# Performance work log

Hardware: AMD Instinct MI355X
Metric: run time of the kernel (lower is better)

The kernel has to match this reference:

```python
import jax, jax.numpy as jnp
import numpy as np

IN_C, HID, L, NN, BS, OUT = 32, 128, 4, 64, 512, 3
N = NN * BS  # total graph vertices
EPS_LN = 1e-5
EPS_SM = 1e-16  # PyG softmax eps


def setup_inputs() -> dict:
    key = jax.random.key(0)
    ks = jax.random.split(key, 16)
    E = 524288
    x = jax.random.normal(ks[0], (N, IN_C), dtype=jnp.float32)
    edge_index = jax.random.randint(ks[1], (2, E), 0, N, dtype=jnp.int64)
    s = 0.1
    # first GAT layer (in -> hidden)
    W0 = jax.random.normal(ks[2], (IN_C, HID), dtype=jnp.float32) * s
    att_src0 = jax.random.normal(ks[3], (HID,), dtype=jnp.float32) * s
    att_dst0 = jax.random.normal(ks[4], (HID,), dtype=jnp.float32) * s
    bias0 = jnp.zeros((HID,), dtype=jnp.float32)
    # residual GAT layers (hidden -> hidden), stacked over L
    W_res = jax.random.normal(ks[5], (L, HID, HID), dtype=jnp.float32) * s
    att_src_res = jax.random.normal(ks[6], (L, HID), dtype=jnp.float32) * s
    att_dst_res = jax.random.normal(ks[7], (L, HID), dtype=jnp.float32) * s
    bias_res = jnp.zeros((L, HID), dtype=jnp.float32)
    gamma = jnp.ones((L, HID), dtype=jnp.float32)
    beta = jnp.zeros((L, HID), dtype=jnp.float32)
    # per-node predictor heads
    W1p = jax.random.normal(ks[8], (NN, HID, HID // 2), dtype=jnp.float32) * s
    W2p = jax.random.normal(ks[9], (NN, HID // 2, OUT), dtype=jnp.float32) * s
    return {"x": x, "edge_index": edge_index, "W0": W0, "att_src0": att_src0,
            "att_dst0": att_dst0, "bias0": bias0, "W_res": W_res,
            "att_src_res": att_src_res, "att_dst_res": att_dst_res,
            "bias_res": bias_res, "gamma": gamma, "beta": beta,
            "W1p": W1p, "W2p": W2p}


def _gat(x, src, dst, W, a_src, a_dst, b):
    # PyG GATConv, heads=1, negative_slope=0.2, self-loops already appended
    h = x @ W                                   # [N, H]
    a_s = (h * a_src).sum(-1)                   # [N]
    a_d = (h * a_dst).sum(-1)                   # [N]
    e = jax.nn.leaky_relu(a_s[src] + a_d[dst], 0.2)   # [E]
    m = jax.ops.segment_max(e, dst, num_segments=N)
    e = jnp.exp(e - m[dst])
    z = jax.ops.segment_sum(e, dst, num_segments=N)
    alpha = e / (z[dst] + EPS_SM)               # [E]
    out = jax.ops.segment_sum(h[src] * alpha[:, None], dst, num_segments=N)
    return out + b


def _layernorm(x, g, b):
    mu = x.mean(-1, keepdims=True)
    var = ((x - mu) ** 2).mean(-1, keepdims=True)
    return (x - mu) * jax.lax.rsqrt(var + EPS_LN) * g + b


def reference(x, edge_index, W0, att_src0, att_dst0, bias0, W_res,
              att_src_res, att_dst_res, bias_res, gamma, beta, W1p, W2p):
    loops = jnp.arange(N, dtype=edge_index.dtype)
    src = jnp.concatenate([edge_index[0], loops])
    dst = jnp.concatenate([edge_index[1], loops])
    # first GAT + relu
    h = jax.nn.relu(_gat(x, src, dst, W0, att_src0, att_dst0, bias0))
    # res+ blocks: h = h + conv(dropout(act(norm(h))))  (dropout=identity, eval)
    for i in range(L):
        t = jax.nn.relu(_layernorm(h, gamma[i], beta[i]))
        t = _gat(t, src, dst, W_res[i], att_src_res[i], att_dst_res[i], bias_res[i])
        h = h + t
    h = jax.nn.relu(_layernorm(h, gamma[0], beta[0]))
    # per-node predictor heads
    h = h.reshape(NN, BS, HID)
    t = jax.nn.relu(jnp.einsum('nbh,nhk->nbk', h, W1p))
    logits = jnp.einsum('nbk,nko->nbo', t, W2p)
    return jax.nn.softmax(logits, axis=-1)   # softmax over class dim (dim=1 per node slice)
```

## Files before the change

### kernel.cpp

```cpp
#include <hip/hip_runtime.h>
#include <hip/hip_fp8.h>
#include <math.h>

#define NND   32768
#define HIDD  128
#define NHEAD 64
#define BSS   512
#define OUTC  3

typedef _Float16 half_t;
typedef __attribute__((ext_vector_type(8))) _Float16 half8;
typedef __attribute__((ext_vector_type(4))) float f32x4;

__device__ __forceinline__ unsigned enc_fp8x4(float a, float b, float c, float d) {
    __hip_fp8x4_e4m3 q(make_float4(a, b, c, d));
    return (unsigned)q.__x;
}
__device__ __forceinline__ float4 dec_fp8x4(unsigned v) {
    __hip_fp8x4_e4m3 t; t.__x = (__hip_fp8x4_storage_t)v;
    return (float4)t;
}

__global__ __launch_bounds__(256) void prep_kernel(const float* __restrict__ W0,
        const float* __restrict__ W_res, const float* __restrict__ W1p,
        const float* __restrict__ as0, const float* __restrict__ ad0,
        const float* __restrict__ as_res, const float* __restrict__ ad_res,
        const float* __restrict__ x, const int* __restrict__ ei, int E,
        half_t* __restrict__ Wh, half_t* __restrict__ W1h, half_t* __restrict__ W0t,
        float* __restrict__ wvec, half_t* __restrict__ xh,
        int* __restrict__ counts, int* __restrict__ rank) {
    int b = blockIdx.x, tid = threadIdx.x;
    if (b < 64) {
        __shared__ float tile[32][33];
        int l = b >> 4, t = b & 15;
        int k0 = (t >> 2) * 32, n0 = (t & 3) * 32;
        const float* src = W_res + (size_t)l * 128 * 128;
        half_t* dst = Wh + (size_t)l * 128 * 128;
        int c = tid & 31, r0 = tid >> 5;
#pragma unroll
        for (int i = 0; i < 4; ++i) tile[r0 + i * 8][c] = src[(size_t)(k0 + r0 + i * 8) * 128 + n0 + c];
        __syncthreads();
#pragma unroll
        for (int i = 0; i < 4; ++i) dst[(size_t)(n0 + r0 + i * 8) * 128 + k0 + c] = (half_t)tile[c][r0 + i * 8];
    } else if (b < 576) {
        __shared__ float tile[32][33];
        int bb = b - 64, head = bb >> 3, t = bb & 7;
        int k0 = (t >> 1) * 32, n0 = (t & 1) * 32;
        const float* src = W1p + (size_t)head * 128 * 64;
        half_t* dst = W1h + (size_t)head * 64 * 128;
        int c = tid & 31, r0 = tid >> 5;
#pragma unroll
        for (int i = 0; i < 4; ++i) tile[r0 + i * 8][c] = src[(size_t)(k0 + r0 + i * 8) * 64 + n0 + c];
        __syncthreads();
#pragma unroll
        for (int i = 0; i < 4; ++i) dst[(size_t)(n0 + r0 + i * 8) * 128 + k0 + c] = (half_t)tile[c][r0 + i * 8];
    } else if (b == 576) {
        __shared__ float t0[32][129];
        for (int i = tid; i < 4096; i += 256) t0[i >> 7][i & 127] = W0[i];
        __syncthreads();
        for (int i = tid; i < 4096; i += 256) { int n = i >> 5, k = i & 31; W0t[n * 32 + k] = (half_t)t0[k][n]; }
    } else if (b == 577) {
        for (int task = tid; task < 1088; task += 256) {
            const float* row; const float* att; int slot, sd;
            if (task < 64) {
                int k = task >> 1; sd = task & 1;
                row = W0 + k * 128; att = sd ? ad0 : as0; slot = k;
            } else {
                int tt = task - 64; int l = 1 + tt / 256; int r = tt % 256;
                int k = r >> 1; sd = r & 1;
                row = W_res + (size_t)(l - 1) * 16384 + k * 128;
                att = (sd ? ad_res : as_res) + (l - 1) * 128;
                slot = l * 128 + k;
            }
            float s = 0.f;
            for (int n = 0; n < 128; ++n) s += row[n] * att[n];
            (sd ? wvec + 640 : wvec)[slot] = s;
        }
    } else if (b < 1090) {
        int b2 = b - 578;
        const float* xs = x + (size_t)b2 * 64 * 32;
        half_t* xd = xh + (size_t)b2 * 64 * 32;
        for (int i = tid; i < 1024; i += 256) {
            float2 v = ((const float2*)xs)[i];
            union { unsigned u; half_t h[2]; } cv;
            cv.h[0] = (half_t)v.x; cv.h[1] = (half_t)v.y;
            ((unsigned*)xd)[i] = cv.u;
        }
    } else {
        int j = (b - 1090) * 256 + tid;
        int Etot = E + NND;
        if (j >= Etot) return;
        int dst = (j < E) ? ei[E + j] : (j - E);
        rank[j] = atomicAdd(&counts[dst], 1);
    }
}

__global__ __launch_bounds__(1024) void scan_kernel(const int* __restrict__ counts,
                                                    int* __restrict__ off) {
    __shared__ int sums[1024];
    int tid = threadIdx.x;
    int base = tid * 32;
    int tmp[32];
    int run = 0;
#pragma unroll
    for (int i = 0; i < 8; ++i) {
        int4 c4 = *(const int4*)&counts[base + i * 4];
        tmp[i*4+0] = run; run += c4.x;
        tmp[i*4+1] = run; run += c4.y;
        tmp[i*4+2] = run; run += c4.z;
        tmp[i*4+3] = run; run += c4.w;
    }
    sums[tid] = run;
    __syncthreads();
    for (int d = 1; d < 1024; d <<= 1) {
        int v = (tid >= d) ? sums[tid - d] : 0;
        __syncthreads();
        sums[tid] += v;
        __syncthreads();
    }
    int ebase = (tid == 0) ? 0 : sums[tid - 1];
#pragma unroll
    for (int i = 0; i < 32; ++i) off[base + i] = ebase + tmp[i];
    if (tid == 1023) off[NND] = sums[1023];
}

__global__ __launch_bounds__(256) void fill_a0_kernel(const int* __restrict__ ei, int E, int egrid,
        const int* __restrict__ off, const int* __restrict__ rank, int* __restrict__ csr_src,
        const half_t* __restrict__ xh, const float* __restrict__ wvec,
        float* __restrict__ a_s, float* __restrict__ a_d) {
    int b = blockIdx.x, tid = threadIdx.x;
    if (b < egrid) {
        int j = b * 256 + tid;
        int Etot = E + NND;
        if (j >= Etot) return;
        int src, dst;
        if (j < E) { src = ei[j]; dst = ei[E + j]; }
        else       { src = j - E; dst = j - E; }
        csr_src[off[dst] + rank[j]] = src;
    } else {
        __shared__ float ws0[32], wd0[32];
        if (tid < 32) { ws0[tid] = wvec[tid]; wd0[tid] = wvec[640 + tid]; }
        __syncthreads();
        int g = (b - egrid) * 256 + tid;
        int node = g >> 2, part = g & 3;
        half8 xv = *(const half8*)&xh[(size_t)node * 32 + part * 8];
        float s = 0.f, d2 = 0.f;
#pragma unroll
        for (int j = 0; j < 8; ++j) { float f = (float)xv[j]; s += f * ws0[part * 8 + j]; d2 += f * wd0[part * 8 + j]; }
        s += __shfl_xor(s, 1); s += __shfl_xor(s, 2);
        d2 += __shfl_xor(d2, 1); d2 += __shfl_xor(d2, 2);
        if (part == 0) { a_s[node] = s; a_d[node] = d2; }
    }
}

__global__ __launch_bounds__(256) void agg0_kernel(const half_t* __restrict__ xh,
        const float* __restrict__ a_s, const float* __restrict__ a_dv,
        const int* __restrict__ csr_src, const int* __restrict__ off,
        half_t* __restrict__ P) {
    int d = (blockIdx.x * 256 + threadIdx.x) >> 6;
    int lane = threadIdx.x & 63;
    int q = lane >> 4, r15 = lane & 15;
    int beg = off[d], end = off[d + 1];
    float adv = a_dv[d];
    float pz = 0.f, a0 = 0.f, a1 = 0.f;
    for (int base = beg; base < end; base += 64) {
        int j = base + lane;
        int s = 0; float p = 0.f;
        if (j < end) {
            s = csr_src[j];
            float t = a_s[s] + adv;
            t = (t > 0.f) ? t : 0.2f * t;
            p = __expf(t);
        }
        pz += p;
        int cnt = end - base; if (cnt > 64) cnt = 64;
        int full = cnt & ~15;
        int k4 = 0;
        for (; k4 < full; k4 += 16) {
            int s0 = __shfl(s, k4 + q);      float p0 = __shfl(p, k4 + q);
            int s1 = __shfl(s, k4 + 4 + q);  float p1 = __shfl(p, k4 + 4 + q);
            int s2 = __shfl(s, k4 + 8 + q);  float p2 = __shfl(p, k4 + 8 + q);
            int s3 = __shfl(s, k4 + 12 + q); float p3 = __shfl(p, k4 + 12 + q);
            union { unsigned u; half_t h[2]; } u0, u1, u2, u3;
            u0.u = *(const unsigned*)&xh[(size_t)s0 * 32 + r15 * 2];
            u1.u = *(const unsigned*)&xh[(size_t)s1 * 32 + r15 * 2];
            u2.u = *(const unsigned*)&xh[(size_t)s2 * 32 + r15 * 2];
            u3.u = *(const unsigned*)&xh[(size_t)s3 * 32 + r15 * 2];
            a0 += p0 * (float)u0.h[0] + p1 * (float)u1.h[0] + p2 * (float)u2.h[0] + p3 * (float)u3.h[0];
            a1 += p0 * (float)u0.h[1] + p1 * (float)u1.h[1] + p2 * (float)u2.h[1] + p3 * (float)u3.h[1];
        }
        for (; k4 < cnt; k4 += 4) {
            int s0 = __shfl(s, k4 + q); float p0 = __shfl(p, k4 + q);
            union { unsigned u; half_t h[2]; } u0;
            u0.u = *(const unsigned*)&xh[(size_t)s0 * 32 + r15 * 2];
            a0 += p0 * (float)u0.h[0]; a1 += p0 * (float)u0.h[1];
        }
    }
#pragma unroll
    for (int o = 32; o; o >>= 1) pz += __shfl_xor(pz, o);
    a0 += __shfl_xor(a0, 16); a0 += __shfl_xor(a0, 32);
    a1 += __shfl_xor(a1, 16); a1 += __shfl_xor(a1, 32);
    if (q == 0) {
        float inv = 1.f / (pz + 1e-16f);
        union { unsigned u; half_t h[2]; } w;
        w.h[0] = (half_t)(a0 * inv); w.h[1] = (half_t)(a1 * inv);
        *(unsigned*)&P[(size_t)d * 32 + r15 * 2] = w.u;
    }
}

__global__ __launch_bounds__(256) void agg_kernel(const unsigned char* __restrict__ F8,
        const float* __restrict__ a_s, const float* __restrict__ a_dv,
        const int* __restrict__ csr_src, const int* __restrict__ off,
        half_t* __restrict__ P) {
    int d = (blockIdx.x * 256 + threadIdx.x) >> 6;
    int lane = threadIdx.x & 63;
    int q = lane >> 4, r15 = lane & 15;
    int beg = off[d], end = off[d + 1];
    float adv = a_dv[d];
    float pz = 0.f;
    float acc[8] = {0.f,0.f,0.f,0.f,0.f,0.f,0.f,0.f};
    for (int base = beg; base < end; base += 64) {
        int j = base + lane;
        int s = 0; float p = 0.f;
        if (j < end) {
            s = csr_src[j];
            float t = a_s[s] + adv;
            t = (t > 0.f) ? t : 0.2f * t;
            p = __expf(t);
        }
        pz += p;
        int cnt = end - base; if (cnt > 64) cnt = 64;
        int full = cnt & ~15;
        int k4 = 0;
        for (; k4 < full; k4 += 16) {
            int s0 = __shfl(s, k4 + q);      float p0 = __shfl(p, k4 + q);
            int s1 = __shfl(s, k4 + 4 + q);  float p1 = __shfl(p, k4 + 4 + q);
            int s2 = __shfl(s, k4 + 8 + q);  float p2 = __shfl(p, k4 + 8 + q);
            int s3 = __shfl(s, k4 + 12 + q); float p3 = __shfl(p, k4 + 12 + q);
            uint2 r0 = *(const uint2*)&F8[(size_t)s0 * HIDD + r15 * 8];
            uint2 r1 = *(const uint2*)&F8[(size_t)s1 * HIDD + r15 * 8];
            uint2 r2 = *(const uint2*)&F8[(size_t)s2 * HIDD + r15 * 8];
            uint2 r3 = *(const uint2*)&F8[(size_t)s3 * HIDD + r15 * 8];
            float4 f;
            f = dec_fp8x4(r0.x); acc[0]+=p0*f.x; acc[1]+=p0*f.y; acc[2]+=p0*f.z; acc[3]+=p0*f.w;
            f = dec_fp8x4(r0.y); acc[4]+=p0*f.x; acc[5]+=p0*f.y; acc[6]+=p0*f.z; acc[7]+=p0*f.w;
            f = dec_fp8x4(r1.x); acc[0]+=p1*f.x; acc[1]+=p1*f.y; acc[2]+=p1*f.z; acc[3]+=p1*f.w;
            f = dec_fp8x4(r1.y); acc[4]+=p1*f.x; acc[5]+=p1*f.y; acc[6]+=p1*f.z; acc[7]+=p1*f.w;
            f = dec_fp8x4(r2.x); acc[0]+=p2*f.x; acc[1]+=p2*f.y; acc[2]+=p2*f.z; acc[3]+=p2*f.w;
            f = dec_fp8x4(r2.y); acc[4]+=p2*f.x; acc[5]+=p2*f.y; acc[6]+=p2*f.z; acc[7]+=p2*f.w;
            f = dec_fp8x4(r3.x); acc[0]+=p3*f.x; acc[1]+=p3*f.y; acc[2]+=p3*f.z; acc[3]+=p3*f.w;
            f = dec_fp8x4(r3.y); acc[4]+=p3*f.x; acc[5]+=p3*f.y; acc[6]+=p3*f.z; acc[7]+=p3*f.w;
        }
        for (; k4 < cnt; k4 += 4) {
            int s0 = __shfl(s, k4 + q); float p0 = __shfl(p, k4 + q);
            uint2 r0 = *(const uint2*)&F8[(size_t)s0 * HIDD + r15 * 8];
            float4 f;
            f = dec_fp8x4(r0.x); acc[0]+=p0*f.x; acc[1]+=p0*f.y; acc[2]+=p0*f.z; acc[3]+=p0*f.w;
            f = dec_fp8x4(r0.y); acc[4]+=p0*f.x; acc[5]+=p0*f.y; acc[6]+=p0*f.z; acc[7]+=p0*f.w;
        }
    }
#pragma unroll
    for (int o = 32; o; o >>= 1) pz += __shfl_xor(pz, o);
#pragma unroll
    for (int i = 0; i < 8; ++i) {
        acc[i] += __shfl_xor(acc[i], 16);
        acc[i] += __shfl_xor(acc[i], 32);
    }
    if (q == 0) {
        float inv = 1.f / (pz + 1e-16f);
        union { int4 v; half_t hh[8]; } u;
#pragma unroll
        for (int i = 0; i < 8; ++i) u.hh[i] = (half_t)(acc[i] * inv);
        *(int4*)&P[(size_t)d * HIDD + r15 * 8] = u.v;
    }
}

template <int K, bool RES>
__global__ __launch_bounds__(256) void gemm_kernel(const half_t* __restrict__ P,
        const half_t* __restrict__ Whl, const float* __restrict__ bias,
        half_t* __restrict__ Hh, unsigned char* __restrict__ Th8,
        const float* __restrict__ gamma, const float* __restrict__ beta,
        const float* __restrict__ wsn, const float* __restrict__ wdn,
        float* __restrict__ a_s, float* __restrict__ a_d) {
    constexpr int KP = K + 8;
    constexpr int WB = 128 * KP * 2;
    constexpr int VB = 64 * 132 * 4;
    __shared__ __align__(16) char smraw[(WB > VB) ? WB : VB];
    half_t* w = (half_t*)smraw;
    float* vv = (float*)smraw;
    int tid = threadIdx.x;
    int n0 = blockIdx.x * 64;
    for (int i = tid; i < 128 * (K / 8); i += 256) {
        int n = i / (K / 8), c = i % (K / 8);
        *(int4*)&w[n * KP + c * 8] = *(const int4*)&Whl[(size_t)n * K + c * 8];
    }
    int wv = tid >> 6, lane = tid & 63;
    int q = lane >> 4, r15 = lane & 15;
    half8 afrag[K / 32];
    int nodeA = n0 + wv * 16 + r15;
#pragma unroll
    for (int s = 0; s < K / 32; ++s)
        afrag[s] = *(const half8*)&P[(size_t)nodeA * K + s * 32 + q * 8];
    __syncthreads();
    f32x4 acc[8];
#pragma unroll
    for (int ct = 0; ct < 8; ++ct) {
        f32x4 c = {0.f, 0.f, 0.f, 0.f};
#pragma unroll
        for (int s = 0; s < K / 32; ++s) {
            half8 bfrag = *(const half8*)&w[(ct * 16 + r15) * KP + s * 32 + q * 8];
            c = __builtin_amdgcn_mfma_f32_16x16x32_f16(afrag[s], bfrag, c, 0, 0, 0);
        }
        acc[ct] = c;
    }
    __syncthreads();
#pragma unroll
    for (int ct = 0; ct < 8; ++ct)
#pragma unroll
        for (int r = 0; r < 4; ++r)
            vv[(wv * 16 + q * 4 + r) * 132 + ct * 16 + r15] = acc[ct][r];
    __syncthreads();
    int grp = tid >> 4, sub = tid & 15;
    float4 bi0 = *(const float4*)&bias[sub * 8],  bi1 = *(const float4*)&bias[sub * 8 + 4];
    float4 g0  = *(const float4*)&gamma[sub * 8], g1  = *(const float4*)&gamma[sub * 8 + 4];
    float4 be0 = *(const float4*)&beta[sub * 8],  be1 = *(const float4*)&beta[sub * 8 + 4];
    float4 ws0 = *(const float4*)&wsn[sub * 8],   ws1 = *(const float4*)&wsn[sub * 8 + 4];
    float4 wd0 = *(const float4*)&wdn[sub * 8],   wd1 = *(const float4*)&wdn[sub * 8 + 4];
    float bi[8] = {bi0.x,bi0.y,bi0.z,bi0.w,bi1.x,bi1.y,bi1.z,bi1.w};
    float gg[8] = {g0.x,g0.y,g0.z,g0.w,g1.x,g1.y,g1.z,g1.w};
    float be[8] = {be0.x,be0.y,be0.z,be0.w,be1.x,be1.y,be1.z,be1.w};
    float ws[8] = {ws0.x,ws0.y,ws0.z,ws0.w,ws1.x,ws1.y,ws1.z,ws1.w};
    float wd[8] = {wd0.x,wd0.y,wd0.z,wd0.w,wd1.x,wd1.y,wd1.z,wd1.w};
#pragma unroll
    for (int pp = 0; pp < 4; ++pp) {
        int nl = grp + pp * 16;
        int node = n0 + nl;
        float v8[8];
#pragma unroll
        for (int j = 0; j < 8; ++j) v8[j] = vv[nl * 132 + sub * 8 + j] + bi[j];
        if (RES) {
            half8 hold = *(const half8*)&Hh[(size_t)node * HIDD + sub * 8];
#pragma unroll
            for (int j = 0; j < 8; ++j) v8[j] += (float)hold[j];
        } else {
#pragma unroll
            for (int j = 0; j < 8; ++j) v8[j] = fmaxf(v8[j], 0.f);
        }
        union { int4 i4; half_t h[8]; } hw;
#pragma unroll
        for (int j = 0; j < 8; ++j) hw.h[j] = (half_t)v8[j];
        *(int4*)&Hh[(size_t)node * HIDD + sub * 8] = hw.i4;
        float sum = 0.f;
#pragma unroll
        for (int j = 0; j < 8; ++j) sum += v8[j];
#pragma unroll
        for (int o = 8; o; o >>= 1) sum += __shfl_xor(sum, o);
        float mu = sum * (1.f / HIDD);
        float var = 0.f;
#pragma unroll
        for (int j = 0; j < 8; ++j) { float dx = v8[j] - mu; var += dx * dx; }
#pragma unroll
        for (int o = 8; o; o >>= 1) var += __shfl_xor(var, o);
        float rs = rsqrtf(var * (1.f / HIDD) + 1e-5f);
        float tt[8];
        float asn = 0.f, adn = 0.f;
#pragma unroll
        for (int j = 0; j < 8; ++j) {
            float t = fmaxf((v8[j] - mu) * rs * gg[j] + be[j], 0.f);
            tt[j] = t;
            asn += t * ws[j];
            adn += t * wd[j];
        }
        uint2 tw;
        tw.x = enc_fp8x4(tt[0], tt[1], tt[2], tt[3]);
        tw.y = enc_fp8x4(tt[4], tt[5], tt[6], tt[7]);
        *(uint2*)&Th8[(size_t)node * HIDD + sub * 8] = tw;
#pragma unroll
        for (int o = 8; o; o >>= 1) { asn += __shfl_xor(asn, o); adn += __shfl_xor(adn, o); }
        if (sub == 0) { a_s[node] = asn; a_d[node] = adn; }
    }
}

__global__ __launch_bounds__(256) void gemm_last_kernel(const half_t* __restrict__ P,
        const half_t* __restrict__ Whl, const float* __restrict__ bias,
        const half_t* __restrict__ Hh,
        const float* __restrict__ gamma, const float* __restrict__ beta,
        const half_t* __restrict__ W1h, const float* __restrict__ W2p,
        float* __restrict__ out) {
    __shared__ __align__(16) char smraw[128 * 136 * 2];
    half_t* w = (half_t*)smraw;
    float* vv = (float*)smraw;
    int tid = threadIdx.x;
    int n0 = blockIdx.x * 64;
    for (int i = tid; i < 128 * 16; i += 256) {
        int n = i >> 4, c = i & 15;
        *(int4*)&w[n * 136 + c * 8] = *(const int4*)&Whl[(size_t)n * 128 + c * 8];
    }
    int wv = tid >> 6, lane = tid & 63;
    int q = lane >> 4, r15 = lane & 15;
    half8 afrag[4];
    int nodeA = n0 + wv * 16 + r15;
#pragma unroll
    for (int s = 0; s < 4; ++s)
        afrag[s] = *(const half8*)&P[(size_t)nodeA * HIDD + s * 32 + q * 8];
    __syncthreads();
    f32x4 acc[8];
#pragma unroll
    for (int ct = 0; ct < 8; ++ct) {
        f32x4 c = {0.f, 0.f, 0.f, 0.f};
#pragma unroll
        for (int s = 0; s < 4; ++s) {
            half8 bfrag = *(const half8*)&w[(ct * 16 + r15) * 136 + s * 32 + q * 8];
            c = __builtin_amdgcn_mfma_f32_16x16x32_f16(afrag[s], bfrag, c, 0, 0, 0);
        }
        acc[ct] = c;
    }
    __syncthreads();
#pragma unroll
    for (int ct = 0; ct < 8; ++ct)
#pragma unroll
        for (int r = 0; r < 4; ++r)
            vv[(wv * 16 + q * 4 + r) * 132 + ct * 16 + r15] = acc[ct][r];
    __syncthreads();
    int grp = tid >> 4, sub = tid & 15;
    float4 bi0 = *(const float4*)&bias[sub * 8],  bi1 = *(const float4*)&bias[sub * 8 + 4];
    float4 g0  = *(const float4*)&gamma[sub * 8], g1  = *(const float4*)&gamma[sub * 8 + 4];
    float4 be0 = *(const float4*)&beta[sub * 8],  be1 = *(const float4*)&beta[sub * 8 + 4];
    float bi[8] = {bi0.x,bi0.y,bi0.z,bi0.w,bi1.x,bi1.y,bi1.z,bi1.w};
    float gg[8] = {g0.x,g0.y,g0.z,g0.w,g1.x,g1.y,g1.z,g1.w};
    float be[8] = {be0.x,be0.y,be0.z,be0.w,be1.x,be1.y,be1.z,be1.w};
    half_t tv[4][8];
#pragma unroll
    for (int pp = 0; pp < 4; ++pp) {
        int nl = grp + pp * 16;
        int node = n0 + nl;
        float v8[8];
        half8 hold = *(const half8*)&Hh[(size_t)node * HIDD + sub * 8];
#pragma unroll
        for (int j = 0; j < 8; ++j) v8[j] = vv[nl * 132 + sub * 8 + j] + bi[j] + (float)hold[j];
        float sum = 0.f;
#pragma unroll
        for (int j = 0; j < 8; ++j) sum += v8[j];
#pragma unroll
        for (int o = 8; o; o >>= 1) sum += __shfl_xor(sum, o);
        float mu = sum * (1.f / HIDD);
        float var = 0.f;
#pragma unroll
        for (int j = 0; j < 8; ++j) { float dx = v8[j] - mu; var += dx * dx; }
#pragma unroll
        for (int o = 8; o; o >>= 1) var += __shfl_xor(var, o);
        float rs = rsqrtf(var * (1.f / HIDD) + 1e-5f);
#pragma unroll
        for (int j = 0; j < 8; ++j)
            tv[pp][j] = (half_t)fmaxf((v8[j] - mu) * rs * gg[j] + be[j], 0.f);
    }
    __syncthreads();
#pragma unroll
    for (int pp = 0; pp < 4; ++pp) {
        int nl = grp + pp * 16;
        union { int4 i4; half_t h[8]; } u;
#pragma unroll
        for (int j = 0; j < 8; ++j) u.h[j] = tv[pp][j];
        *(int4*)&w[nl * 136 + sub * 8] = u.i4;
    }
    __syncthreads();
    int head = n0 >> 9;
    const half_t* W1g = W1h + (size_t)head * 64 * 128;
    half8 pa[4];
#pragma unroll
    for (int s = 0; s < 4; ++s)
        pa[s] = *(const half8*)&w[(wv * 16 + r15) * 136 + s * 32 + q * 8];
    float lg[3][4];
#pragma unroll
    for (int o = 0; o < 3; ++o)
#pragma unroll
        for (int r = 0; r < 4; ++r) lg[o][r] = 0.f;
#pragma unroll
    for (int ct2 = 0; ct2 < 4; ++ct2) {
        int n2 = ct2 * 16 + r15;
        f32x4 c = {0.f, 0.f, 0.f, 0.f};
#pragma unroll
        for (int s = 0; s < 4; ++s) {
            half8 bfrag = *(const half8*)&W1g[(size_t)n2 * 128 + s * 32 + q * 8];
            c = __builtin_amdgcn_mfma_f32_16x16x32_f16(pa[s], bfrag, c, 0, 0, 0);
        }
        float w2a = W2p[(size_t)head * 192 + n2 * 3 + 0];
        float w2b = W2p[(size_t)head * 192 + n2 * 3 + 1];
        float w2c = W2p[(size_t)head * 192 + n2 * 3 + 2];
#pragma unroll
        for (int r = 0; r < 4; ++r) {
            float t = fmaxf(c[r], 0.f);
            lg[0][r] += t * w2a;
            lg[1][r] += t * w2b;
            lg[2][r] += t * w2c;
        }
    }
#pragma unroll
    for (int o = 8; o; o >>= 1)
#pragma unroll
        for (int oo = 0; oo < 3; ++oo)
#pragma unroll
            for (int r = 0; r < 4; ++r) lg[oo][r] += __shfl_xor(lg[oo][r], o);
    if (r15 == 0) {
        int nodeD = n0 + wv * 16 + q * 4;
#pragma unroll
        for (int r = 0; r < 4; ++r) {
            float l0 = lg[0][r], l1 = lg[1][r], l2 = lg[2][r];
            float mx = fmaxf(l0, fmaxf(l1, l2));
            float e0 = __expf(l0 - mx), e1 = __expf(l1 - mx), e2 = __expf(l2 - mx);
            float inv = 1.f / (e0 + e1 + e2);
            float* op = out + (size_t)(nodeD + r) * OUTC;
            op[0] = e0 * inv; op[1] = e1 * inv; op[2] = e2 * inv;
        }
    }
}

extern "C" void kernel_launch(void* const* d_in, const int* in_sizes, int n_in,
                              void* d_out, int out_size, void* d_ws, size_t ws_size,
                              hipStream_t stream) {
    const float* x        = (const float*)d_in[0];
    const int*   ei       = (const int*)d_in[1];
    const float* W0       = (const float*)d_in[2];
    const float* att_src0 = (const float*)d_in[3];
    const float* att_dst0 = (const float*)d_in[4];
    const float* bias0    = (const float*)d_in[5];
    const float* W_res    = (const float*)d_in[6];
    const float* as_res   = (const float*)d_in[7];
    const float* ad_res   = (const float*)d_in[8];
    const float* b_res    = (const float*)d_in[9];
    const float* gamma    = (const float*)d_in[10];
    const float* beta     = (const float*)d_in[11];
    const float* W1p      = (const float*)d_in[12];
    const float* W2p      = (const float*)d_in[13];
    float* out = (float*)d_out;

    int E = in_sizes[1] / 2;
    int Etot = E + NND;

    char* p = (char*)d_ws;
    auto alloc = [&](size_t bytes) { void* r = (void*)p; p += (bytes + 255) & ~(size_t)255; return r; };
    int*    counts  = (int*)alloc((size_t)NND * 4);
    int*    off     = (int*)alloc((size_t)(NND + 1) * 4);
    int*    rank    = (int*)alloc((size_t)Etot * 4);
    int*    csr_src = (int*)alloc((size_t)Etot * 4);
    half_t* xh      = (half_t*)alloc((size_t)NND * 32 * 2);
    half_t* Pbuf    = (half_t*)alloc((size_t)NND * HIDD * 2);
    unsigned char* Th8 = (unsigned char*)alloc((size_t)NND * HIDD);
    half_t* Hh      = (half_t*)alloc((size_t)NND * HIDD * 2);
    float*  a_s     = (float*)alloc((size_t)NND * 4);
    float*  a_d     = (float*)alloc((size_t)NND * 4);
    half_t* Wh      = (half_t*)alloc((size_t)4 * HIDD * HIDD * 2);
    half_t* W1h     = (half_t*)alloc((size_t)NHEAD * 64 * HIDD * 2);
    half_t* W0t     = (half_t*)alloc((size_t)HIDD * 32 * 2);
    float*  wvec    = (float*)alloc((size_t)1280 * 4);

    int egrid = (Etot + 255) / 256;

    hipMemsetAsync(counts, 0, (size_t)NND * 4, stream);
    prep_kernel<<<1090 + egrid, 256, 0, stream>>>(W0, W_res, W1p, att_src0, att_dst0,
        as_res, ad_res, x, ei, E, Wh, W1h, W0t, wvec, xh, counts, rank);
    scan_kernel<<<1, 1024, 0, stream>>>(counts, off);
    fill_a0_kernel<<<egrid + 512, 256, 0, stream>>>(ei, E, egrid, off, rank, csr_src,
                                                    xh, wvec, a_s, a_d);

    agg0_kernel<<<NND / 4, 256, 0, stream>>>(xh, a_s, a_d, csr_src, off, Pbuf);
    gemm_kernel<32, false><<<NND / 64, 256, 0, stream>>>(Pbuf, W0t, bias0, Hh, Th8,
        gamma, beta, wvec + 128, wvec + 640 + 128, a_s, a_d);

    for (int i = 0; i < 3; ++i) {
        agg_kernel<<<NND / 4, 256, 0, stream>>>(Th8, a_s, a_d, csr_src, off, Pbuf);
        gemm_kernel<128, true><<<NND / 64, 256, 0, stream>>>(Pbuf, Wh + (size_t)i * 16384,
            b_res + i * HIDD, Hh, Th8,
            gamma + (i + 1) * HIDD, beta + (i + 1) * HIDD,
            wvec + (i + 2) * 128, wvec + 640 + (i + 2) * 128, a_s, a_d);
    }

    agg_kernel<<<NND / 4, 256, 0, stream>>>(Th8, a_s, a_d, csr_src, off, Pbuf);
    gemm_last_kernel<<<NND / 64, 256, 0, stream>>>(Pbuf, Wh + (size_t)3 * 16384,
        b_res + 3 * HIDD, Hh, gamma, beta, W1h, W2p, out);
}
```

Baseline: 280.7 us.

## Fuse GAT aggregation with GEMM/LayerNorm epilogue per 16-node block

Merges the edge-softmax aggregation and the following dense GEMM plus residual/LayerNorm/attention-score epilogue into one kernel. Each block aggregates 16 destination nodes into shared memory and then runs MFMA directly on them, so the P intermediate never goes through global memory and the per-layer launch count is halved. Because a block now reads features and scores produced by the previous layer while writing new ones, the fp8 features and the a_s/a_d buffers are double-buffered. Trade-offs: weights are read straight from global memory (L2) by every 16-node block rather than staged in LDS, the blocks are smaller, and each wave processes 4 nodes one after another, which may reduce memory-level parallelism in the gather.

```diff
diff --git a/kernel.cpp b/kernel.cpp
--- a/kernel.cpp
+++ b/kernel.cpp
@@ -153,59 +153,213 @@
     }
 }
 
-__global__ __launch_bounds__(256) void agg0_kernel(const half_t* __restrict__ xh,
-        const float* __restrict__ a_s, const float* __restrict__ a_dv,
+template <int K, bool RES>
+__global__ __launch_bounds__(256) void fused_kernel(const void* __restrict__ srcdat,
+        const float* __restrict__ a_sv, const float* __restrict__ a_dv,
         const int* __restrict__ csr_src, const int* __restrict__ off,
-        half_t* __restrict__ P) {
-    int d = (blockIdx.x * 256 + threadIdx.x) >> 6;
-    int lane = threadIdx.x & 63;
+        const half_t* __restrict__ Whl, const float* __restrict__ bias,
+        half_t* __restrict__ Hh, unsigned char* __restrict__ Th8o,
+        const float* __restrict__ gamma, const float* __restrict__ beta,
+        const float* __restrict__ wsn, const float* __restrict__ wdn,
+        float* __restrict__ as_out, float* __restrict__ ad_out) {
+    constexpr int KP = (K == 32) ? 40 : 136;
+    __shared__ __align__(16) half_t Pt[16][KP];
+    __shared__ __align__(16) float vv[16][132];
+    int tid = threadIdx.x;
+    int wv = tid >> 6, lane = tid & 63;
     int q = lane >> 4, r15 = lane & 15;
-    int beg = off[d], end = off[d + 1];
-    float adv = a_dv[d];
-    float pz = 0.f, a0 = 0.f, a1 = 0.f;
-    for (int base = beg; base < end; base += 64) {
-        int j = base + lane;
-        int s = 0; float p = 0.f;
-        if (j < end) {
-            s = csr_src[j];
-            float t = a_s[s] + adv;
-            t = (t > 0.f) ? t : 0.2f * t;
-            p = __expf(t);
-        }
-        pz += p;
-        int cnt = end - base; if (cnt > 64) cnt = 64;
-        int full = cnt & ~15;
-        int k4 = 0;
-        for (; k4 < full; k4 += 16) {
-            int s0 = __shfl(s, k4 + q);      float p0 = __shfl(p, k4 + q);
-            int s1 = __shfl(s, k4 + 4 + q);  float p1 = __shfl(p, k4 + 4 + q);
-            int s2 = __shfl(s, k4 + 8 + q);  float p2 = __shfl(p, k4 + 8 + q);
-            int s3 = __shfl(s, k4 + 12 + q); float p3 = __shfl(p, k4 + 12 + q);
-            union { unsigned u; half_t h[2]; } u0, u1, u2, u3;
-            u0.u = *(const unsigned*)&xh[(size_t)s0 * 32 + r15 * 2];
-            u1.u = *(const unsigned*)&xh[(size_t)s1 * 32 + r15 * 2];
-            u2.u = *(const unsigned*)&xh[(size_t)s2 * 32 + r15 * 2];
-            u3.u = *(const unsigned*)&xh[(size_t)s3 * 32 + r15 * 2];
-            a0 += p0 * (float)u0.h[0] + p1 * (float)u1.h[0] + p2 * (float)u2.h[0] + p3 * (float)u3.h[0];
-            a1 += p0 * (float)u0.h[1] + p1 * (float)u1.h[1] + p2 * (float)u2.h[1] + p3 * (float)u3.h[1];
-        }
-        for (; k4 < cnt; k4 += 4) {
-            int s0 = __shfl(s, k4 + q); float p0 = __shfl(p, k4 + q);
-            union { unsigned u; half_t h[2]; } u0;
-            u0.u = *(const unsigned*)&xh[(size_t)s0 * 32 + r15 * 2];
-            a0 += p0 * (float)u0.h[0]; a1 += p0 * (float)u0.h[1];
-        }
-    }
-#pragma unroll
-    for (int o = 32; o; o >>= 1) pz += __shfl_xor(pz, o);
-    a0 += __shfl_xor(a0, 16); a0 += __shfl_xor(a0, 32);
-    a1 += __shfl_xor(a1, 16); a1 += __shfl_xor(a1, 32);
-    if (q == 0) {
-        float inv = 1.f / (pz + 1e-16f);
-        union { unsigned u; half_t h[2]; } w;
-        w.h[0] = (half_t)(a0 * inv); w.h[1] = (half_t)(a1 * inv);
-        *(unsigned*)&P[(size_t)d * 32 + r15 * 2] = w.u;
-    }
+    int n0 = blockIdx.x * 16;
+
+    for (int ln = wv * 4; ln < wv * 4 + 4; ++ln) {
+        int d = n0 + ln;
+        int beg = off[d], end = off[d + 1];
+        float adv = a_dv[d];
+        float pz = 0.f;
+        if constexpr (K == 32) {
+            const half_t* xh = (const half_t*)srcdat;
+            float a0 = 0.f, a1 = 0.f;
+            for (int base = beg; base < end; base += 64) {
+                int j = base + lane;
+                int s = 0; float p = 0.f;
+                if (j < end) {
+                    s = csr_src[j];
+                    float t = a_sv[s] + adv;
+                    t = (t > 0.f) ? t : 0.2f * t;
+                    p = __expf(t);
+                }
+                pz += p;
+                int cnt = end - base; if (cnt > 64) cnt = 64;
+                int full = cnt & ~15;
+                int k4 = 0;
+                for (; k4 < full; k4 += 16) {
+                    int s0 = __shfl(s, k4 + q);      float p0 = __shfl(p, k4 + q);
+                    int s1 = __shfl(s, k4 + 4 + q);  float p1 = __shfl(p, k4 + 4 + q);
+                    int s2 = __shfl(s, k4 + 8 + q);  float p2 = __shfl(p, k4 + 8 + q);
+                    int s3 = __shfl(s, k4 + 12 + q); float p3 = __shfl(p, k4 + 12 + q);
+                    union { unsigned u; half_t h[2]; } u0, u1, u2, u3;
+                    u0.u = *(const unsigned*)&xh[(size_t)s0 * 32 + r15 * 2];
+                    u1.u = *(const unsigned*)&xh[(size_t)s1 * 32 + r15 * 2];
+                    u2.u = *(const unsigned*)&xh[(size_t)s2 * 32 + r15 * 2];
+                    u3.u = *(const unsigned*)&xh[(size_t)s3 * 32 + r15 * 2];
+                    a0 += p0 * (float)u0.h[0] + p1 * (float)u1.h[0] + p2 * (float)u2.h[0] + p3 * (float)u3.h[0];
+                    a1 += p0 * (float)u0.h[1] + p1 * (float)u1.h[1] + p2 * (float)u2.h[1] + p3 * (float)u3.h[1];
+                }
+                for (; k4 < cnt; k4 += 4) {
+                    int s0 = __shfl(s, k4 + q); float p0 = __shfl(p, k4 + q);
+                    union { unsigned u; half_t h[2]; } u0;
+                    u0.u = *(const unsigned*)&xh[(size_t)s0 * 32 + r15 * 2];
+                    a0 += p0 * (float)u0.h[0]; a1 += p0 * (float)u0.h[1];
+                }
+            }
+#pragma unroll
+            for (int o = 32; o; o >>= 1) pz += __shfl_xor(pz, o);
+            a0 += __shfl_xor(a0, 16); a0 += __shfl_xor(a0, 32);
+            a1 += __shfl_xor(a1, 16); a1 += __shfl_xor(a1, 32);
+            if (q == 0) {
+                float inv = 1.f / (pz + 1e-16f);
+                union { unsigned u; half_t h[2]; } w2;
+                w2.h[0] = (half_t)(a0 * inv); w2.h[1] = (half_t)(a1 * inv);
+                *(unsigned*)&Pt[ln][r15 * 2] = w2.u;
+            }
+        } else {
+            const unsigned char* F8 = (const unsigned char*)srcdat;
+            float acc[8] = {0.f,0.f,0.f,0.f,0.f,0.f,0.f,0.f};
+            for (int base = beg; base < end; base += 64) {
+                int j = base + lane;
+                int s = 0; float p = 0.f;
+                if (j < end) {
+                    s = csr_src[j];
+                    float t = a_sv[s] + adv;
+                    t = (t > 0.f) ? t : 0.2f * t;
+                    p = __expf(t);
+                }
+                pz += p;
+                int cnt = end - base; if (cnt > 64) cnt = 64;
+                int full = cnt & ~15;
+                int k4 = 0;
+                for (; k4 < full; k4 += 16) {
+                    int s0 = __shfl(s, k4 + q);      float p0 = __shfl(p, k4 + q);
+                    int s1 = __shfl(s, k4 + 4 + q);  float p1 = __shfl(p, k4 + 4 + q);
+                    int s2 = __shfl(s, k4 + 8 + q);  float p2 = __shfl(p, k4 + 8 + q);
+                    int s3 = __shfl(s, k4 + 12 + q); float p3 = __shfl(p, k4 + 12 + q);
+                    uint2 r0 = *(const uint2*)&F8[(size_t)s0 * HIDD + r15 * 8];
+                    uint2 r1 = *(const uint2*)&F8[(size_t)s1 * HIDD + r15 * 8];
+                    uint2 r2 = *(const uint2*)&F8[(size_t)s2 * HIDD + r15 * 8];
+                    uint2 r3 = *(const uint2*)&F8[(size_t)s3 * HIDD + r15 * 8];
+                    float4 f;
+                    f = dec_fp8x4(r0.x); acc[0]+=p0*f.x; acc[1]+=p0*f.y; acc[2]+=p0*f.z; acc[3]+=p0*f.w;
+                    f = dec_fp8x4(r0.y); acc[4]+=p0*f.x; acc[5]+=p0*f.y; acc[6]+=p0*f.z; acc[7]+=p0*f.w;
+                    f = dec_fp8x4(r1.x); acc[0]+=p1*f.x; acc[1]+=p1*f.y; acc[2]+=p1*f.z; acc[3]+=p1*f.w;
+                    f = dec_fp8x4(r1.y); acc[4]+=p1*f.x; acc[5]+=p1*f.y; acc[6]+=p1*f.z; acc[7]+=p1*f.w;
+                    f = dec_fp8x4(r2.x); acc[0]+=p2*f.x; acc[1]+=p2*f.y; acc[2]+=p2*f.z; acc[3]+=p2*f.w;
+                    f = dec_fp8x4(r2.y); acc[4]+=p2*f.x; acc[5]+=p2*f.y; acc[6]+=p2*f.z; acc[7]+=p2*f.w;
+                    f = dec_fp8x4(r3.x); acc[0]+=p3*f.x; acc[1]+=p3*f.y; acc[2]+=p3*f.z; acc[3]+=p3*f.w;
+                    f = dec_fp8x4(r3.y); acc[4]+=p3*f.x; acc[5]+=p3*f.y; acc[6]+=p3*f.z; acc[7]+=p3*f.w;
+                }
+                for (; k4 < cnt; k4 += 4) {
+                    int s0 = __shfl(s, k4 + q); float p0 = __shfl(p, k4 + q);
+                    uint2 r0 = *(const uint2*)&F8[(size_t)s0 * HIDD + r15 * 8];
+                    float4 f;
+                    f = dec_fp8x4(r0.x); acc[0]+=p0*f.x; acc[1]+=p0*f.y; acc[2]+=p0*f.z; acc[3]+=p0*f.w;
+                    f = dec_fp8x4(r0.y); acc[4]+=p0*f.x; acc[5]+=p0*f.y; acc[6]+=p0*f.z; acc[7]+=p0*f.w;
+                }
+            }
+#pragma unroll
+            for (int o = 32; o; o >>= 1) pz += __shfl_xor(pz, o);
+#pragma unroll
+            for (int i = 0; i < 8; ++i) {
+                acc[i] += __shfl_xor(acc[i], 16);
+                acc[i] += __shfl_xor(acc[i], 32);
+            }
+            if (q == 0) {
+                float inv = 1.f / (pz + 1e-16f);
+                union { int4 v; half_t hh[8]; } u;
+#pragma unroll
+                for (int i = 0; i < 8; ++i) u.hh[i] = (half_t)(acc[i] * inv);
+                *(int4*)&Pt[ln][r15 * 8] = u.v;
+            }
+        }
+    }
+    __syncthreads();
+
+    half8 afrag[K / 32];
+#pragma unroll
+    for (int s = 0; s < K / 32; ++s)
+        afrag[s] = *(const half8*)&Pt[r15][s * 32 + q * 8];
+    f32x4 acc2[2];
+#pragma unroll
+    for (int i = 0; i < 2; ++i) {
+        int ct = wv * 2 + i;
+        f32x4 c = {0.f, 0.f, 0.f, 0.f};
+#pragma unroll
+        for (int s = 0; s < K / 32; ++s) {
+            half8 bfrag = *(const half8*)&Whl[(size_t)(ct * 16 + r15) * K + s * 32 + q * 8];
+            c = __builtin_amdgcn_mfma_f32_16x16x32_f16(afrag[s], bfrag, c, 0, 0, 0);
+        }
+        acc2[i] = c;
+    }
+#pragma unroll
+    for (int i = 0; i < 2; ++i)
+#pragma unroll
+        for (int r = 0; r < 4; ++r)
+            vv[q * 4 + r][wv * 32 + i * 16 + r15] = acc2[i][r];
+    __syncthreads();
+
+    int grp = tid >> 4, sub = tid & 15;
+    float4 bi0 = *(const float4*)&bias[sub * 8],  bi1 = *(const float4*)&bias[sub * 8 + 4];
+    float4 g0  = *(const float4*)&gamma[sub * 8], g1  = *(const float4*)&gamma[sub * 8 + 4];
+    float4 be0 = *(const float4*)&beta[sub * 8],  be1 = *(const float4*)&beta[sub * 8 + 4];
+    float4 ws0 = *(const float4*)&wsn[sub * 8],   ws1 = *(const float4*)&wsn[sub * 8 + 4];
+    float4 wd0 = *(const float4*)&wdn[sub * 8],   wd1 = *(const float4*)&wdn[sub * 8 + 4];
+    float bi[8] = {bi0.x,bi0.y,bi0.z,bi0.w,bi1.x,bi1.y,bi1.z,bi1.w};
+    float gg[8] = {g0.x,g0.y,g0.z,g0.w,g1.x,g1.y,g1.z,g1.w};
+    float be[8] = {be0.x,be0.y,be0.z,be0.w,be1.x,be1.y,be1.z,be1.w};
+    float ws[8] = {ws0.x,ws0.y,ws0.z,ws0.w,ws1.x,ws1.y,ws1.z,ws1.w};
+    float wd[8] = {wd0.x,wd0.y,wd0.z,wd0.w,wd1.x,wd1.y,wd1.z,wd1.w};
+    int node = n0 + grp;
+    float v8[8];
+#pragma unroll
+    for (int j = 0; j < 8; ++j) v8[j] = vv[grp][sub * 8 + j] + bi[j];
+    if (RES) {
+        half8 hold = *(const half8*)&Hh[(size_t)node * HIDD + sub * 8];
+#pragma unroll
+        for (int j = 0; j < 8; ++j) v8[j] += (float)hold[j];
+    } else {
+#pragma unroll
+        for (int j = 0; j < 8; ++j) v8[j] = fmaxf(v8[j], 0.f);
+    }
+    union { int4 i4; half_t h[8]; } hw;
+#pragma unroll
+    for (int j = 0; j < 8; ++j) hw.h[j] = (half_t)v8[j];
+    *(int4*)&Hh[(size_t)node * HIDD + sub * 8] = hw.i4;
+    float sum = 0.f;
+#pragma unroll
+    for (int j = 0; j < 8; ++j) sum += v8[j];
+#pragma unroll
+    for (int o = 8; o; o >>= 1) sum += __shfl_xor(sum, o);
+    float mu = sum * (1.f / HIDD);
+    float var = 0.f;
+#pragma unroll
+    for (int j = 0; j < 8; ++j) { float dx = v8[j] - mu; var += dx * dx; }
+#pragma unroll
+    for (int o = 8; o; o >>= 1) var += __shfl_xor(var, o);
+    float rs = rsqrtf(var * (1.f / HIDD) + 1e-5f);
+    float tt[8];
+    float asn = 0.f, adn = 0.f;
+#pragma unroll
+    for (int j = 0; j < 8; ++j) {
+        float t = fmaxf((v8[j] - mu) * rs * gg[j] + be[j], 0.f);
+        tt[j] = t;
+        asn += t * ws[j];
+        adn += t * wd[j];
+    }
+    uint2 tw;
+    tw.x = enc_fp8x4(tt[0], tt[1], tt[2], tt[3]);
+    tw.y = enc_fp8x4(tt[4], tt[5], tt[6], tt[7]);
+    *(uint2*)&Th8o[(size_t)node * HIDD + sub * 8] = tw;
+#pragma unroll
+    for (int o = 8; o; o >>= 1) { asn += __shfl_xor(asn, o); adn += __shfl_xor(adn, o); }
+    if (sub == 0) { as_out[node] = asn; ad_out[node] = adn; }
 }
 
 __global__ __launch_bounds__(256) void agg_kernel(const unsigned char* __restrict__ F8,
@@ -275,112 +429,6 @@
     }
 }
 
-template <int K, bool RES>
-__global__ __launch_bounds__(256) void gemm_kernel(const half_t* __restrict__ P,
-        const half_t* __restrict__ Whl, const float* __restrict__ bias,
-        half_t* __restrict__ Hh, unsigned char* __restrict__ Th8,
-        const float* __restrict__ gamma, const float* __restrict__ beta,
-        const float* __restrict__ wsn, const float* __restrict__ wdn,
-        float* __restrict__ a_s, float* __restrict__ a_d) {
-    constexpr int KP = K + 8;
-    constexpr int WB = 128 * KP * 2;
-    constexpr int VB = 64 * 132 * 4;
-    __shared__ __align__(16) char smraw[(WB > VB) ? WB : VB];
-    half_t* w = (half_t*)smraw;
-    float* vv = (float*)smraw;
-    int tid = threadIdx.x;
-    int n0 = blockIdx.x * 64;
-    for (int i = tid; i < 128 * (K / 8); i += 256) {
-        int n = i / (K / 8), c = i % (K / 8);
-        *(int4*)&w[n * KP + c * 8] = *(const int4*)&Whl[(size_t)n * K + c * 8];
-    }
-    int wv = tid >> 6, lane = tid & 63;
-    int q = lane >> 4, r15 = lane & 15;
-    half8 afrag[K / 32];
-    int nodeA = n0 + wv * 16 + r15;
-#pragma unroll
-    for (int s = 0; s < K / 32; ++s)
-        afrag[s] = *(const half8*)&P[(size_t)nodeA * K + s * 32 + q * 8];
-    __syncthreads();
-    f32x4 acc[8];
-#pragma unroll
-    for (int ct = 0; ct < 8; ++ct) {
-        f32x4 c = {0.f, 0.f, 0.f, 0.f};
-#pragma unroll
-        for (int s = 0; s < K / 32; ++s) {
-            half8 bfrag = *(const half8*)&w[(ct * 16 + r15) * KP + s * 32 + q * 8];
-            c = __builtin_amdgcn_mfma_f32_16x16x32_f16(afrag[s], bfrag, c, 0, 0, 0);
-        }
-        acc[ct] = c;
-    }
-    __syncthreads();
-#pragma unroll
-    for (int ct = 0; ct < 8; ++ct)
-#pragma unroll
-        for (int r = 0; r < 4; ++r)
-            vv[(wv * 16 + q * 4 + r) * 132 + ct * 16 + r15] = acc[ct][r];
-    __syncthreads();
-    int grp = tid >> 4, sub = tid & 15;
-    float4 bi0 = *(const float4*)&bias[sub * 8],  bi1 = *(const float4*)&bias[sub * 8 + 4];
-    float4 g0  = *(const float4*)&gamma[sub * 8], g1  = *(const float4*)&gamma[sub * 8 + 4];
-    float4 be0 = *(const float4*)&beta[sub * 8],  be1 = *(const float4*)&beta[sub * 8 + 4];
-    float4 ws0 = *(const float4*)&wsn[sub * 8],   ws1 = *(const float4*)&wsn[sub * 8 + 4];
-    float4 wd0 = *(const float4*)&wdn[sub * 8],   wd1 = *(const float4*)&wdn[sub * 8 + 4];
-    float bi[8] = {bi0.x,bi0.y,bi0.z,bi0.w,bi1.x,bi1.y,bi1.z,bi1.w};
-    float gg[8] = {g0.x,g0.y,g0.z,g0.w,g1.x,g1.y,g1.z,g1.w};
-    float be[8] = {be0.x,be0.y,be0.z,be0.w,be1.x,be1.y,be1.z,be1.w};
-    float ws[8] = {ws0.x,ws0.y,ws0.z,ws0.w,ws1.x,ws1.y,ws1.z,ws1.w};
-    float wd[8] = {wd0.x,wd0.y,wd0.z,wd0.w,wd1.x,wd1.y,wd1.z,wd1.w};
-#pragma unroll
-    for (int pp = 0; pp < 4; ++pp) {
-        int nl = grp + pp * 16;
-        int node = n0 + nl;
-        float v8[8];
-#pragma unroll
-        for (int j = 0; j < 8; ++j) v8[j] = vv[nl * 132 + sub * 8 + j] + bi[j];
-        if (RES) {
-            half8 hold = *(const half8*)&Hh[(size_t)node * HIDD + sub * 8];
-#pragma unroll
-            for (int j = 0; j < 8; ++j) v8[j] += (float)hold[j];
-        } else {
-#pragma unroll
-            for (int j = 0; j < 8; ++j) v8[j] = fmaxf(v8[j], 0.f);
-        }
-        union { int4 i4; half_t h[8]; } hw;
-#pragma unroll
-        for (int j = 0; j < 8; ++j) hw.h[j] = (half_t)v8[j];
-        *(int4*)&Hh[(size_t)node * HIDD + sub * 8] = hw.i4;
-        float sum = 0.f;
-#pragma unroll
-        for (int j = 0; j < 8; ++j) sum += v8[j];
-#pragma unroll
-        for (int o = 8; o; o >>= 1) sum += __shfl_xor(sum, o);
-        float mu = sum * (1.f / HIDD);
-        float var = 0.f;
-#pragma unroll
-        for (int j = 0; j < 8; ++j) { float dx = v8[j] - mu; var += dx * dx; }
-#pragma unroll
-        for (int o = 8; o; o >>= 1) var += __shfl_xor(var, o);
-        float rs = rsqrtf(var * (1.f / HIDD) + 1e-5f);
-        float tt[8];
-        float asn = 0.f, adn = 0.f;
-#pragma unroll
-        for (int j = 0; j < 8; ++j) {
-            float t = fmaxf((v8[j] - mu) * rs * gg[j] + be[j], 0.f);
-            tt[j] = t;
-            asn += t * ws[j];
-            adn += t * wd[j];
-        }
-        uint2 tw;
-        tw.x = enc_fp8x4(tt[0], tt[1], tt[2], tt[3]);
-        tw.y = enc_fp8x4(tt[4], tt[5], tt[6], tt[7]);
-        *(uint2*)&Th8[(size_t)node * HIDD + sub * 8] = tw;
-#pragma unroll
-        for (int o = 8; o; o >>= 1) { asn += __shfl_xor(asn, o); adn += __shfl_xor(adn, o); }
-        if (sub == 0) { a_s[node] = asn; a_d[node] = adn; }
-    }
-}
-
 __global__ __launch_bounds__(256) void gemm_last_kernel(const half_t* __restrict__ P,
         const half_t* __restrict__ Whl, const float* __restrict__ bias,
         const half_t* __restrict__ Hh,
@@ -545,10 +593,13 @@
     int*    csr_src = (int*)alloc((size_t)Etot * 4);
     half_t* xh      = (half_t*)alloc((size_t)NND * 32 * 2);
     half_t* Pbuf    = (half_t*)alloc((size_t)NND * HIDD * 2);
-    unsigned char* Th8 = (unsigned char*)alloc((size_t)NND * HIDD);
+    unsigned char* Th8a = (unsigned char*)alloc((size_t)NND * HIDD);
+    unsigned char* Th8b = (unsigned char*)alloc((size_t)NND * HIDD);
     half_t* Hh      = (half_t*)alloc((size_t)NND * HIDD * 2);
-    float*  a_s     = (float*)alloc((size_t)NND * 4);
-    float*  a_d     = (float*)alloc((size_t)NND * 4);
+    float*  a_s0    = (float*)alloc((size_t)NND * 4);
+    float*  a_d0    = (float*)alloc((size_t)NND * 4);
+    float*  a_s1    = (float*)alloc((size_t)NND * 4);
+    float*  a_d1    = (float*)alloc((size_t)NND * 4);
     half_t* Wh      = (half_t*)alloc((size_t)4 * HIDD * HIDD * 2);
     half_t* W1h     = (half_t*)alloc((size_t)NHEAD * 64 * HIDD * 2);
     half_t* W0t     = (half_t*)alloc((size_t)HIDD * 32 * 2);
@@ -561,21 +612,23 @@
         as_res, ad_res, x, ei, E, Wh, W1h, W0t, wvec, xh, counts, rank);
     scan_kernel<<<1, 1024, 0, stream>>>(counts, off);
     fill_a0_kernel<<<egrid + 512, 256, 0, stream>>>(ei, E, egrid, off, rank, csr_src,
-                                                    xh, wvec, a_s, a_d);
-
-    agg0_kernel<<<NND / 4, 256, 0, stream>>>(xh, a_s, a_d, csr_src, off, Pbuf);
-    gemm_kernel<32, false><<<NND / 64, 256, 0, stream>>>(Pbuf, W0t, bias0, Hh, Th8,
-        gamma, beta, wvec + 128, wvec + 640 + 128, a_s, a_d);
-
-    for (int i = 0; i < 3; ++i) {
-        agg_kernel<<<NND / 4, 256, 0, stream>>>(Th8, a_s, a_d, csr_src, off, Pbuf);
-        gemm_kernel<128, true><<<NND / 64, 256, 0, stream>>>(Pbuf, Wh + (size_t)i * 16384,
-            b_res + i * HIDD, Hh, Th8,
-            gamma + (i + 1) * HIDD, beta + (i + 1) * HIDD,
-            wvec + (i + 2) * 128, wvec + 640 + (i + 2) * 128, a_s, a_d);
-    }
-
-    agg_kernel<<<NND / 4, 256, 0, stream>>>(Th8, a_s, a_d, csr_src, off, Pbuf);
+                                                    xh, wvec, a_s0, a_d0);
+
+    fused_kernel<32, false><<<NND / 16, 256, 0, stream>>>((const void*)xh,
+        a_s0, a_d0, csr_src, off, W0t, bias0, Hh, Th8a,
+        gamma, beta, wvec + 128, wvec + 640 + 128, a_s1, a_d1);
+
+    fused_kernel<128, true><<<NND / 16, 256, 0, stream>>>((const void*)Th8a,
+        a_s1, a_d1, csr_src, off, Wh, b_res, Hh, Th8b,
+        gamma + 128, beta + 128, wvec + 256, wvec + 640 + 256, a_s0, a_d0);
+    fused_kernel<128, true><<<NND / 16, 256, 0, stream>>>((const void*)Th8b,
+        a_s0, a_d0, csr_src, off, Wh + 16384, b_res + 128, Hh, Th8a,
+        gamma + 256, beta + 256, wvec + 384, wvec + 640 + 384, a_s1, a_d1);
+    fused_kernel<128, true><<<NND / 16, 256, 0, stream>>>((const void*)Th8a,
+        a_s1, a_d1, csr_src, off, Wh + 2 * 16384, b_res + 2 * 128, Hh, Th8b,
+        gamma + 384, beta + 384, wvec + 512, wvec + 640 + 512, a_s0, a_d0);
+
+    agg_kernel<<<NND / 4, 256, 0, stream>>>(Th8b, a_s0, a_d0, csr_src, off, Pbuf);
     gemm_last_kernel<<<NND / 64, 256, 0, stream>>>(Pbuf, Wh + (size_t)3 * 16384,
         b_res + 3 * HIDD, Hh, gamma, beta, W1h, W2p, out);
 }
```

Result: no change. 284.4 us (+1.3%).
